# Performance work log

Measured on AMD Instinct MI355X. Metric: run time of the kernel, lower is better.

The kernel has to match this reference:

```python
import jax, jax.numpy as jnp
import numpy as np

B, D, U, C = 2048, 512, 512, 100


def setup_inputs() -> dict:
    key = jax.random.key(0)
    k1, k2, k3 = jax.random.split(key, 3)
    x = jax.random.normal(k1, (B, D), dtype=jnp.float32)
    classes = jax.random.randint(k2, (B, 1), 0, C, dtype=jnp.int64)
    # glorot-uniform-like init for the per-class kernel table
    limit = np.sqrt(6.0 / (D + U)).astype(np.float32)
    kernel = jax.random.uniform(k3, (C, D, U), dtype=jnp.float32, minval=-limit, maxval=limit)
    bias = jnp.zeros((C, U), dtype=jnp.float32)
    return {"x": x, "classes": classes, "kernel": kernel, "bias": bias}


def reference(x, classes, kernel, bias):
    cls = jnp.squeeze(classes, axis=1)            # [B]
    w = kernel[cls]                               # [B, D, U] per-sample gathered kernel
    out = jnp.einsum('bd,bdu->bu', x, w)          # batched matmul, x treated as [B,1,D]
    out = out + bias[cls]                         # per-sample gathered bias
    return out                                    # activation is None (linear)
```

## Files before the change

### kernel.cpp

```cpp
#include <hip/hip_runtime.h>
#include <hip/hip_bf16.h>


typedef __attribute__((ext_vector_type(8))) short bf16x8;
typedef __attribute__((ext_vector_type(4))) short short4v;
typedef __attribute__((ext_vector_type(4))) float floatx4;

constexpr int C_CLS   = 100;
constexpr int B_N     = 2048;
constexpr int D_DIM   = 512;
constexpr int U_DIM   = 512;
constexpr int S_CHUNK = 32;
constexpr int MAX_CHUNKS = 164;
constexpr int TU      = 128;
constexpr int PROWS   = 16;
constexpr int PIECES  = D_DIM / PROWS;
constexpr int NQ      = 4;
constexpr int NWG     = 4 * MAX_CHUNKS;

__device__ __forceinline__ short f2bf(float f) {
    return (short)__builtin_bit_cast(unsigned short, __float2bfloat16(f));
}


__global__ void k_sort(const int* __restrict__ cls, int* __restrict__ order,
                       int* __restrict__ total_chunks, int* __restrict__ chunk_cls,
                       int* __restrict__ chunk_start, int* __restrict__ chunk_len) {
    __shared__ int s_cnt[128], s_off[128], s_chk[128], s_cur[128], s_base[128];
    int tid = threadIdx.x;
    if (tid < 128) s_cnt[tid] = 0;
    __syncthreads();
    for (int i = tid; i < B_N; i += 1024) atomicAdd(&s_cnt[cls[i]], 1);
    __syncthreads();
    int cnt = 0, nch = 0;
    if (tid < 128) {
        cnt = (tid < C_CLS) ? s_cnt[tid] : 0;
        nch = (cnt + S_CHUNK - 1) / S_CHUNK;
        s_off[tid] = cnt; s_chk[tid] = nch;
    }
    __syncthreads();
    for (int st = 1; st < 128; st <<= 1) {
        int a = 0, b = 0;
        if (tid >= st && tid < 128) { a = s_off[tid - st]; b = s_chk[tid - st]; }
        __syncthreads();
        if (tid < 128) { s_off[tid] += a; s_chk[tid] += b; }
        __syncthreads();
    }
    if (tid < C_CLS) {
        int off = s_off[tid] - cnt;
        int cb  = s_chk[tid] - nch;
        s_base[tid] = off;
        s_cur[tid]  = 0;
        for (int j = 0; j < nch; ++j) {
            chunk_cls[cb + j]   = tid;
            chunk_start[cb + j] = off + j * S_CHUNK;
            chunk_len[cb + j]   = min(S_CHUNK, cnt - j * S_CHUNK);
        }
    }
    if (tid == 127) *total_chunks = s_chk[127];
    __syncthreads();
    for (int i = tid; i < B_N; i += 1024) {
        int c = cls[i];
        int p = atomicAdd(&s_cur[c], 1);
        order[s_base[c] + p] = i;
    }
}


#define ISSUE(pi, qq) do {                                                    \
    const int db_ = (pi) * PROWS;                                             \
    _Pragma("unroll")                                                         \
    for (int j_ = 0; j_ < 2; ++j_) {                                          \
        const int r_  = wv * 4 + 2 * j_;           \
        const int rr_ = r_ + (lane >> 5);        \
        const float* gp_ = Wg + (size_t)(db_ + rr_) * U_DIM                   \
                           + (((lane & 31) ^ (rr_ & 15)) << 2);               \
        __builtin_amdgcn_global_load_lds(                                     \
            (const __attribute__((address_space(1))) void*)gp_,               \
            (__attribute__((address_space(3))) void*)&wbuf[qq][r_][0],        \
            16, 0, 0);                                                        \
    }                                                                         \
} while (0)

#define COMPUTE(pi, qq) do {                                                  \
    bf16x8 a8_0, a8_1;                                                        \
    {                                                                         \
        const int xb_ = ((pi) * 32 + g4 * 8) ^ sxw_;                          \
        short4v a4 = *reinterpret_cast<const short4v*>(                       \
            (const char*)xsb + sA * 1024 + xb_);                              \
        a8_0[0]=a4[0]; a8_0[1]=a4[1]; a8_0[2]=a4[2]; a8_0[3]=a4[3];           \
        a8_0[4]=a4[0]; a8_0[5]=a4[1]; a8_0[6]=a4[2]; a8_0[7]=a4[3];           \
        short4v a4b = *reinterpret_cast<const short4v*>(                      \
            (const char*)xsb + (16 + sA) * 1024 + xb_);                       \
        a8_1[0]=a4b[0]; a8_1[1]=a4b[1]; a8_1[2]=a4b[2]; a8_1[3]=a4b[3];       \
        a8_1[4]=a4b[0]; a8_1[5]=a4b[1]; a8_1[6]=a4b[2]; a8_1[7]=a4b[3];       \
    }                                                                         \
    const char* wb_ = (const char*)wbuf + (qq) * (PROWS * TU * 4);            \
    _Pragma("unroll")                                                         \
    for (int nt = 0; nt < 2; ++nt) {                                          \
        const int cb4_ = ((wv << 5) + nt * 16 + sA) << 2;                     \
        bf16x8 b8;                                                            \
        _Pragma("unroll")                                                     \
        for (int j_ = 0; j_ < 4; ++j_) {                                      \
            const int rl_ = g4 * 4 + j_;                                      \
            float w_ = *reinterpret_cast<const float*>(                       \
                wb_ + rl_ * 512 + (cb4_ ^ (rl_ << 4)));                       \
            b8[j_] = f2bf(w_);                                                \
        }                                                                     \
        b8[4] = 0; b8[5] = 0; b8[6] = 0; b8[7] = 0;                           \
        acc0[nt] = __builtin_amdgcn_mfma_f32_16x16x32_bf16(a8_0, b8, acc0[nt], 0, 0, 0); \
        acc1[nt] = __builtin_amdgcn_mfma_f32_16x16x32_bf16(a8_1, b8, acc1[nt], 0, 0, 0); \
    }                                                                         \
} while (0)

#define STEP(pi, NCNT) do {                                                   \
    asm volatile("s_waitcnt vmcnt(" #NCNT ")" ::: "memory");                  \
    __builtin_amdgcn_s_barrier();                  \
    COMPUTE(pi, (pi) & 3);                                                    \
    asm volatile("" ::: "memory");                                            \
    __builtin_amdgcn_s_barrier();               \
    if ((pi) + NQ < PIECES) ISSUE((pi) + NQ, (pi) & 3);                       \
} while (0)

__launch_bounds__(256, 2)
__global__ void k_main(const float* __restrict__ x, const float* __restrict__ kern,
                       const float* __restrict__ bias, const int* __restrict__ order,
                       const int* __restrict__ total_chunks,
                       const int* __restrict__ chunk_cls,
                       const int* __restrict__ chunk_start,
                       const int* __restrict__ chunk_len,
                       float* __restrict__ out) {
    int tc = *total_chunks;
    int A  = 4 * tc;
    int xc = blockIdx.x & 7;
    int ii = blockIdx.x >> 3;
    int q  = A >> 3, r = A & 7;
    int mycnt = (xc < r) ? (q + 1) : q;
    if (ii >= mycnt) return;
    int g = ((xc < r) ? xc * (q + 1) : r * (q + 1) + (xc - r) * q) + ii;

    int chunk = g >> 2;
    int ytile = g & 3;

    int tid  = threadIdx.x;
    int lane = tid & 63;
    int wv   = tid >> 6;
    int sA   = lane & 15;
    int g4   = lane >> 4;
    const int sxw_ = (sA & 7) << 4;

    int c     = chunk_cls[chunk];
    int start = chunk_start[chunk];
    int len   = chunk_len[chunk];
    int u0    = ytile * TU;

    __shared__ float          wbuf[NQ][PROWS][TU];
    __shared__ unsigned short xsb[S_CHUNK][D_DIM];
    __shared__ int            sidx[S_CHUNK];

    const float* Wg = kern + (size_t)c * (D_DIM * U_DIM) + u0;

    if (tid < S_CHUNK) sidx[tid] = (tid < len) ? order[start + tid] : -1;
    asm volatile("s_waitcnt lgkmcnt(0)" ::: "memory");
    __builtin_amdgcn_s_barrier();

    float4 xv0[8], xv1[8];
    int srow0 = (tid >> 4), srow1 = 16 + (tid >> 4);
    int cb    = (tid & 15) * 32;
    {
        int b0 = sidx[srow0]; if (b0 < 0) b0 = sidx[0];
        int b1 = sidx[srow1]; if (b1 < 0) b1 = sidx[0];
        #pragma unroll
        for (int j = 0; j < 8; ++j)
            xv0[j] = reinterpret_cast<const float4*>(x + (size_t)b0 * D_DIM + cb)[j];
        #pragma unroll
        for (int j = 0; j < 8; ++j)
            xv1[j] = reinterpret_cast<const float4*>(x + (size_t)b1 * D_DIM + cb)[j];
    }
    ISSUE(0, 0);
    ISSUE(1, 1);
    ISSUE(2, 2);
    ISSUE(3, 3);
    asm volatile("s_waitcnt vmcnt(8)" ::: "memory");

    {
        #pragma unroll
        for (int p = 0; p < 2; ++p) {
            int   row  = p ? srow1 : srow0;
            char* xrow = (char*)xsb + row * 1024;
            int   swz  = (row & 7) << 4;
            #pragma unroll
            for (int m = 0; m < 4; ++m) {
                float4 va = p ? xv1[2*m]     : xv0[2*m];
                float4 vb = p ? xv1[2*m + 1] : xv0[2*m + 1];
                bf16x8 pk;
                pk[0] = f2bf(va.x); pk[1] = f2bf(va.y);
                pk[2] = f2bf(va.z); pk[3] = f2bf(va.w);
                pk[4] = f2bf(vb.x); pk[5] = f2bf(vb.y);
                pk[6] = f2bf(vb.z); pk[7] = f2bf(vb.w);
                *reinterpret_cast<bf16x8*>(xrow + ((cb * 2 + m * 16) ^ swz)) = pk;
            }
        }
    }
    asm volatile("s_waitcnt lgkmcnt(0)" ::: "memory");
    __builtin_amdgcn_s_barrier();

    floatx4 acc0[2], acc1[2];
    #pragma unroll
    for (int k = 0; k < 2; ++k) {
        acc0[k] = (floatx4){0.f, 0.f, 0.f, 0.f};
        acc1[k] = (floatx4){0.f, 0.f, 0.f, 0.f};
    }

    #pragma unroll 1
    for (int i = 0; i <= 27; ++i) STEP(i, 6);
    STEP(28, 6);
    STEP(29, 4);
    STEP(30, 2);
    STEP(31, 0);

    #pragma unroll
    for (int mt = 0; mt < 2; ++mt) {
        #pragma unroll
        for (int nt = 0; nt < 2; ++nt) {
            int u  = u0 + (wv << 5) + nt * 16 + sA;
            float bb = bias[c * U_DIM + u];
            floatx4 a = mt ? acc1[nt] : acc0[nt];
            #pragma unroll
            for (int r2 = 0; r2 < 4; ++r2) {
                int b = sidx[mt * 16 + g4 * 4 + r2];
                if (b >= 0) out[(size_t)b * U_DIM + u] = a[r2] + bb;
            }
        }
    }
}


extern "C" void kernel_launch(void* const* d_in, const int* in_sizes, int n_in,
                              void* d_out, int out_size, void* d_ws, size_t ws_size,
                              hipStream_t stream) {
    const float* x    = (const float*)d_in[0];
    const int*   cls  = (const int*)d_in[1];
    const float* kern = (const float*)d_in[2];
    const float* bias = (const float*)d_in[3];
    float*       out  = (float*)d_out;

    int* ws           = (int*)d_ws;
    int* order        = ws;
    int* total_chunks = ws + 2048;
    int* chunk_cls    = ws + 2112;
    int* chunk_start  = ws + 2304;
    int* chunk_len    = ws + 2496;

    hipLaunchKernelGGL(k_sort, dim3(1), dim3(1024), 0, stream,
                       cls, order, total_chunks, chunk_cls, chunk_start, chunk_len);
    hipLaunchKernelGGL(k_main, dim3(NWG), dim3(256), 0, stream,
                       x, kern, bias, order, total_chunks, chunk_cls, chunk_start, chunk_len, out);
}
```

Measured before the change: 32.41 us.

## Halve U tile to 64 columns, doubling workgroups and raising occupancy

The U tile per workgroup shrinks from 128 to 64 columns, so there are twice as many workgroups per chunk (8 instead of 4) and each wave computes one 16-column MFMA tile instead of two. Weight staging now issues one 16-byte global-to-LDS load per thread per piece without the XOR swizzle, and the vmcnt waits are adjusted to match. The x-row gather is restructured to load and convert one row-half at a time, and launch bounds move to 3 blocks per CU. The intent is more parallelism and occupancy on a bandwidth-bound gather-GEMM. The cost is redundant x loading and conversion per workgroup, and possible LDS bank conflicts from dropping the swizzle.

```diff
diff --git a/kernel.cpp b/kernel.cpp
--- a/kernel.cpp
+++ b/kernel.cpp
@@ -12,11 +12,11 @@
 constexpr int U_DIM   = 512;
 constexpr int S_CHUNK = 32;
 constexpr int MAX_CHUNKS = 164;
-constexpr int TU      = 128;
+constexpr int TU      = 64;
 constexpr int PROWS   = 16;
 constexpr int PIECES  = D_DIM / PROWS;
 constexpr int NQ      = 4;
-constexpr int NWG     = 4 * MAX_CHUNKS;
+constexpr int NWG     = 8 * MAX_CHUNKS;
 
 __device__ __forceinline__ short f2bf(float f) {
     return (short)__builtin_bit_cast(unsigned short, __float2bfloat16(f));
@@ -68,18 +68,13 @@
 
 
 #define ISSUE(pi, qq) do {                                                    \
-    const int db_ = (pi) * PROWS;                                             \
-    _Pragma("unroll")                                                         \
-    for (int j_ = 0; j_ < 2; ++j_) {                                          \
-        const int r_  = wv * 4 + 2 * j_;           \
-        const int rr_ = r_ + (lane >> 5);        \
-        const float* gp_ = Wg + (size_t)(db_ + rr_) * U_DIM                   \
-                           + (((lane & 31) ^ (rr_ & 15)) << 2);               \
-        __builtin_amdgcn_global_load_lds(                                     \
-            (const __attribute__((address_space(1))) void*)gp_,               \
-            (__attribute__((address_space(3))) void*)&wbuf[qq][r_][0],        \
-            16, 0, 0);                                                        \
-    }                                                                         \
+    const int db_ = (pi) * PROWS + 4 * wv;                                    \
+    const float* gp_ = Wg + (size_t)(db_ + (lane >> 4)) * U_DIM               \
+                       + ((lane & 15) << 2);                                  \
+    __builtin_amdgcn_global_load_lds(                                         \
+        (const __attribute__((address_space(1))) void*)gp_,                   \
+        (__attribute__((address_space(3))) void*)&wbuf[qq][4 * wv][0],        \
+        16, 0, 0);                                                            \
 } while (0)
 
 #define COMPUTE(pi, qq) do {                                                  \
@@ -96,20 +91,18 @@
         a8_1[4]=a4b[0]; a8_1[5]=a4b[1]; a8_1[6]=a4b[2]; a8_1[7]=a4b[3];       \
     }                                                                         \
     const char* wb_ = (const char*)wbuf + (qq) * (PROWS * TU * 4);            \
-    _Pragma("unroll")                                                         \
-    for (int nt = 0; nt < 2; ++nt) {                                          \
-        const int cb4_ = ((wv << 5) + nt * 16 + sA) << 2;                     \
+    {                                                                         \
+        const int cb4_ = (wv * 16 + sA) << 2;      \
         bf16x8 b8;                                                            \
         _Pragma("unroll")                                                     \
         for (int j_ = 0; j_ < 4; ++j_) {                                      \
             const int rl_ = g4 * 4 + j_;                                      \
-            float w_ = *reinterpret_cast<const float*>(                       \
-                wb_ + rl_ * 512 + (cb4_ ^ (rl_ << 4)));                       \
+            float w_ = *reinterpret_cast<const float*>(wb_ + rl_ * 256 + cb4_); \
             b8[j_] = f2bf(w_);                                                \
         }                                                                     \
         b8[4] = 0; b8[5] = 0; b8[6] = 0; b8[7] = 0;                           \
-        acc0[nt] = __builtin_amdgcn_mfma_f32_16x16x32_bf16(a8_0, b8, acc0[nt], 0, 0, 0); \
-        acc1[nt] = __builtin_amdgcn_mfma_f32_16x16x32_bf16(a8_1, b8, acc1[nt], 0, 0, 0); \
+        acc0 = __builtin_amdgcn_mfma_f32_16x16x32_bf16(a8_0, b8, acc0, 0, 0, 0); \
+        acc1 = __builtin_amdgcn_mfma_f32_16x16x32_bf16(a8_1, b8, acc1, 0, 0, 0); \
     }                                                                         \
 } while (0)
 
@@ -122,7 +115,7 @@
     if ((pi) + NQ < PIECES) ISSUE((pi) + NQ, (pi) & 3);                       \
 } while (0)
 
-__launch_bounds__(256, 2)
+__launch_bounds__(256, 3)
 __global__ void k_main(const float* __restrict__ x, const float* __restrict__ kern,
                        const float* __restrict__ bias, const int* __restrict__ order,
                        const int* __restrict__ total_chunks,
@@ -131,7 +124,7 @@
                        const int* __restrict__ chunk_len,
                        float* __restrict__ out) {
     int tc = *total_chunks;
-    int A  = 4 * tc;
+    int A  = 8 * tc;
     int xc = blockIdx.x & 7;
     int ii = blockIdx.x >> 3;
     int q  = A >> 3, r = A & 7;
@@ -139,8 +132,8 @@
     if (ii >= mycnt) return;
     int g = ((xc < r) ? xc * (q + 1) : r * (q + 1) + (xc - r) * q) + ii;
 
-    int chunk = g >> 2;
-    int ytile = g & 3;
+    int chunk = g >> 3;
+    int ytile = g & 7;
 
     int tid  = threadIdx.x;
     int lane = tid & 63;
@@ -164,73 +157,54 @@
     asm volatile("s_waitcnt lgkmcnt(0)" ::: "memory");
     __builtin_amdgcn_s_barrier();
 
-    float4 xv0[8], xv1[8];
-    int srow0 = (tid >> 4), srow1 = 16 + (tid >> 4);
-    int cb    = (tid & 15) * 32;
-    {
-        int b0 = sidx[srow0]; if (b0 < 0) b0 = sidx[0];
-        int b1 = sidx[srow1]; if (b1 < 0) b1 = sidx[0];
-        #pragma unroll
-        for (int j = 0; j < 8; ++j)
-            xv0[j] = reinterpret_cast<const float4*>(x + (size_t)b0 * D_DIM + cb)[j];
-        #pragma unroll
-        for (int j = 0; j < 8; ++j)
-            xv1[j] = reinterpret_cast<const float4*>(x + (size_t)b1 * D_DIM + cb)[j];
-    }
+    int srow = tid >> 4;
+    int cb   = (tid & 15) * 32;
     ISSUE(0, 0);
     ISSUE(1, 1);
     ISSUE(2, 2);
     ISSUE(3, 3);
-    asm volatile("s_waitcnt vmcnt(8)" ::: "memory");
-
-    {
+    #pragma unroll
+    for (int p = 0; p < 2; ++p) {
+        int row = p * 16 + srow;
+        int b0 = sidx[row]; if (b0 < 0) b0 = sidx[0];
+        float4 xv[8];
         #pragma unroll
-        for (int p = 0; p < 2; ++p) {
-            int   row  = p ? srow1 : srow0;
-            char* xrow = (char*)xsb + row * 1024;
-            int   swz  = (row & 7) << 4;
-            #pragma unroll
-            for (int m = 0; m < 4; ++m) {
-                float4 va = p ? xv1[2*m]     : xv0[2*m];
-                float4 vb = p ? xv1[2*m + 1] : xv0[2*m + 1];
-                bf16x8 pk;
-                pk[0] = f2bf(va.x); pk[1] = f2bf(va.y);
-                pk[2] = f2bf(va.z); pk[3] = f2bf(va.w);
-                pk[4] = f2bf(vb.x); pk[5] = f2bf(vb.y);
-                pk[6] = f2bf(vb.z); pk[7] = f2bf(vb.w);
-                *reinterpret_cast<bf16x8*>(xrow + ((cb * 2 + m * 16) ^ swz)) = pk;
-            }
+        for (int j = 0; j < 8; ++j)
+            xv[j] = reinterpret_cast<const float4*>(x + (size_t)b0 * D_DIM + cb)[j];
+        asm volatile("s_waitcnt vmcnt(4)" ::: "memory");
+        char* xrow = (char*)xsb + row * 1024;
+        int   swz  = (row & 7) << 4;
+        #pragma unroll
+        for (int m = 0; m < 4; ++m) {
+            bf16x8 pk;
+            pk[0] = f2bf(xv[2*m].x);   pk[1] = f2bf(xv[2*m].y);
+            pk[2] = f2bf(xv[2*m].z);   pk[3] = f2bf(xv[2*m].w);
+            pk[4] = f2bf(xv[2*m+1].x); pk[5] = f2bf(xv[2*m+1].y);
+            pk[6] = f2bf(xv[2*m+1].z); pk[7] = f2bf(xv[2*m+1].w);
+            *reinterpret_cast<bf16x8*>(xrow + ((cb * 2 + m * 16) ^ swz)) = pk;
         }
     }
     asm volatile("s_waitcnt lgkmcnt(0)" ::: "memory");
     __builtin_amdgcn_s_barrier();
 
-    floatx4 acc0[2], acc1[2];
-    #pragma unroll
-    for (int k = 0; k < 2; ++k) {
-        acc0[k] = (floatx4){0.f, 0.f, 0.f, 0.f};
-        acc1[k] = (floatx4){0.f, 0.f, 0.f, 0.f};
-    }
+    floatx4 acc0 = (floatx4){0.f, 0.f, 0.f, 0.f};
+    floatx4 acc1 = (floatx4){0.f, 0.f, 0.f, 0.f};
 
     #pragma unroll 1
-    for (int i = 0; i <= 27; ++i) STEP(i, 6);
-    STEP(28, 6);
-    STEP(29, 4);
-    STEP(30, 2);
+    for (int i = 0; i <= 28; ++i) STEP(i, 3);
+    STEP(29, 2);
+    STEP(30, 1);
     STEP(31, 0);
 
-    #pragma unroll
-    for (int mt = 0; mt < 2; ++mt) {
+    {
+        int u  = u0 + wv * 16 + sA;
+        float bb = bias[c * U_DIM + u];
         #pragma unroll
-        for (int nt = 0; nt < 2; ++nt) {
-            int u  = u0 + (wv << 5) + nt * 16 + sA;
-            float bb = bias[c * U_DIM + u];
-            floatx4 a = mt ? acc1[nt] : acc0[nt];
-            #pragma unroll
-            for (int r2 = 0; r2 < 4; ++r2) {
-                int b = sidx[mt * 16 + g4 * 4 + r2];
-                if (b >= 0) out[(size_t)b * U_DIM + u] = a[r2] + bb;
-            }
+        for (int r2 = 0; r2 < 4; ++r2) {
+            int b0 = sidx[g4 * 4 + r2];
+            if (b0 >= 0) out[(size_t)b0 * U_DIM + u] = acc0[r2] + bb;
+            int b1 = sidx[16 + g4 * 4 + r2];
+            if (b1 >= 0) out[(size_t)b1 * U_DIM + u] = acc1[r2] + bb;
         }
     }
 }
```

Result: slower. 48.49 us (+49.6%).

## Widen output tile to 256 columns with 512-thread workgroups

Applied to the files above, without the earlier changes.

Doubles the per-workgroup U tile from 128 to 256 columns and the block size from 256 to 512 threads, which halves the number of workgroups per chunk. Each workgroup now gathers and converts the x rows for its chunk once for twice as many output columns, so x loads and bf16 conversion are repeated less often. The LDS weight-staging layout and swizzle are reworked for the wider rows. The costs are a larger LDS footprint, one resident block per CU under the new launch bounds, and fewer workgroups to spread across the GPU.

```diff
diff --git a/kernel.cpp b/kernel.cpp
--- a/kernel.cpp
+++ b/kernel.cpp
@@ -12,11 +12,11 @@
 constexpr int U_DIM   = 512;
 constexpr int S_CHUNK = 32;
 constexpr int MAX_CHUNKS = 164;
-constexpr int TU      = 128;
+constexpr int TU      = 256;
 constexpr int PROWS   = 16;
 constexpr int PIECES  = D_DIM / PROWS;
 constexpr int NQ      = 4;
-constexpr int NWG     = 4 * MAX_CHUNKS;
+constexpr int NWG     = 2 * MAX_CHUNKS;
 
 __device__ __forceinline__ short f2bf(float f) {
     return (short)__builtin_bit_cast(unsigned short, __float2bfloat16(f));
@@ -71,13 +71,12 @@
     const int db_ = (pi) * PROWS;                                             \
     _Pragma("unroll")                                                         \
     for (int j_ = 0; j_ < 2; ++j_) {                                          \
-        const int r_  = wv * 4 + 2 * j_;           \
-        const int rr_ = r_ + (lane >> 5);        \
-        const float* gp_ = Wg + (size_t)(db_ + rr_) * U_DIM                   \
-                           + (((lane & 31) ^ (rr_ & 15)) << 2);               \
+        const int row_ = 2 * wv + j_;                                         \
+        const float* gp_ = Wg + (size_t)(db_ + row_) * U_DIM                  \
+                           + ((lane ^ (row_ & 7)) << 2);                      \
         __builtin_amdgcn_global_load_lds(                                     \
             (const __attribute__((address_space(1))) void*)gp_,               \
-            (__attribute__((address_space(3))) void*)&wbuf[qq][r_][0],        \
+            (__attribute__((address_space(3))) void*)&wbuf[qq][row_][0],      \
             16, 0, 0);                                                        \
     }                                                                         \
 } while (0)
@@ -98,13 +97,13 @@
     const char* wb_ = (const char*)wbuf + (qq) * (PROWS * TU * 4);            \
     _Pragma("unroll")                                                         \
     for (int nt = 0; nt < 2; ++nt) {                                          \
-        const int cb4_ = ((wv << 5) + nt * 16 + sA) << 2;                     \
+        const int c_ = (wv << 5) + nt * 16 + sA;        \
         bf16x8 b8;                                                            \
         _Pragma("unroll")                                                     \
         for (int j_ = 0; j_ < 4; ++j_) {                                      \
             const int rl_ = g4 * 4 + j_;                                      \
             float w_ = *reinterpret_cast<const float*>(                       \
-                wb_ + rl_ * 512 + (cb4_ ^ (rl_ << 4)));                       \
+                wb_ + rl_ * 1024 + ((c_ << 2) ^ ((rl_ & 7) << 4)));           \
             b8[j_] = f2bf(w_);                                                \
         }                                                                     \
         b8[4] = 0; b8[5] = 0; b8[6] = 0; b8[7] = 0;                           \
@@ -115,14 +114,14 @@
 
 #define STEP(pi, NCNT) do {                                                   \
     asm volatile("s_waitcnt vmcnt(" #NCNT ")" ::: "memory");                  \
-    __builtin_amdgcn_s_barrier();                  \
+    __builtin_amdgcn_s_barrier();                                             \
     COMPUTE(pi, (pi) & 3);                                                    \
     asm volatile("" ::: "memory");                                            \
-    __builtin_amdgcn_s_barrier();               \
+    __builtin_amdgcn_s_barrier();                                             \
     if ((pi) + NQ < PIECES) ISSUE((pi) + NQ, (pi) & 3);                       \
 } while (0)
 
-__launch_bounds__(256, 2)
+__launch_bounds__(512, 1)
 __global__ void k_main(const float* __restrict__ x, const float* __restrict__ kern,
                        const float* __restrict__ bias, const int* __restrict__ order,
                        const int* __restrict__ total_chunks,
@@ -131,7 +130,7 @@
                        const int* __restrict__ chunk_len,
                        float* __restrict__ out) {
     int tc = *total_chunks;
-    int A  = 4 * tc;
+    int A  = 2 * tc;
     int xc = blockIdx.x & 7;
     int ii = blockIdx.x >> 3;
     int q  = A >> 3, r = A & 7;
@@ -139,8 +138,8 @@
     if (ii >= mycnt) return;
     int g = ((xc < r) ? xc * (q + 1) : r * (q + 1) + (xc - r) * q) + ii;
 
-    int chunk = g >> 2;
-    int ytile = g & 3;
+    int chunk = g >> 1;
+    int ytile = g & 1;
 
     int tid  = threadIdx.x;
     int lane = tid & 63;
@@ -164,18 +163,14 @@
     asm volatile("s_waitcnt lgkmcnt(0)" ::: "memory");
     __builtin_amdgcn_s_barrier();
 
-    float4 xv0[8], xv1[8];
-    int srow0 = (tid >> 4), srow1 = 16 + (tid >> 4);
-    int cb    = (tid & 15) * 32;
+    int srow = tid >> 4;
+    int cb   = (tid & 15) * 32;
+    float4 xv[8];
     {
-        int b0 = sidx[srow0]; if (b0 < 0) b0 = sidx[0];
-        int b1 = sidx[srow1]; if (b1 < 0) b1 = sidx[0];
+        int b0 = sidx[srow]; if (b0 < 0) b0 = sidx[0];
         #pragma unroll
         for (int j = 0; j < 8; ++j)
-            xv0[j] = reinterpret_cast<const float4*>(x + (size_t)b0 * D_DIM + cb)[j];
-        #pragma unroll
-        for (int j = 0; j < 8; ++j)
-            xv1[j] = reinterpret_cast<const float4*>(x + (size_t)b1 * D_DIM + cb)[j];
+            xv[j] = reinterpret_cast<const float4*>(x + (size_t)b0 * D_DIM + cb)[j];
     }
     ISSUE(0, 0);
     ISSUE(1, 1);
@@ -184,22 +179,16 @@
     asm volatile("s_waitcnt vmcnt(8)" ::: "memory");
 
     {
+        char* xrow = (char*)xsb + srow * 1024;
+        int   swz  = (srow & 7) << 4;
         #pragma unroll
-        for (int p = 0; p < 2; ++p) {
-            int   row  = p ? srow1 : srow0;
-            char* xrow = (char*)xsb + row * 1024;
-            int   swz  = (row & 7) << 4;
-            #pragma unroll
-            for (int m = 0; m < 4; ++m) {
-                float4 va = p ? xv1[2*m]     : xv0[2*m];
-                float4 vb = p ? xv1[2*m + 1] : xv0[2*m + 1];
-                bf16x8 pk;
-                pk[0] = f2bf(va.x); pk[1] = f2bf(va.y);
-                pk[2] = f2bf(va.z); pk[3] = f2bf(va.w);
-                pk[4] = f2bf(vb.x); pk[5] = f2bf(vb.y);
-                pk[6] = f2bf(vb.z); pk[7] = f2bf(vb.w);
-                *reinterpret_cast<bf16x8*>(xrow + ((cb * 2 + m * 16) ^ swz)) = pk;
-            }
+        for (int m = 0; m < 4; ++m) {
+            bf16x8 pk;
+            pk[0] = f2bf(xv[2*m].x);   pk[1] = f2bf(xv[2*m].y);
+            pk[2] = f2bf(xv[2*m].z);   pk[3] = f2bf(xv[2*m].w);
+            pk[4] = f2bf(xv[2*m+1].x); pk[5] = f2bf(xv[2*m+1].y);
+            pk[6] = f2bf(xv[2*m+1].z); pk[7] = f2bf(xv[2*m+1].w);
+            *reinterpret_cast<bf16x8*>(xrow + ((cb * 2 + m * 16) ^ swz)) = pk;
         }
     }
     asm volatile("s_waitcnt lgkmcnt(0)" ::: "memory");
@@ -254,6 +243,6 @@
 
     hipLaunchKernelGGL(k_sort, dim3(1), dim3(1024), 0, stream,
                        cls, order, total_chunks, chunk_cls, chunk_start, chunk_len);
-    hipLaunchKernelGGL(k_main, dim3(NWG), dim3(256), 0, stream,
+    hipLaunchKernelGGL(k_main, dim3(NWG), dim3(512), 0, stream,
                        x, kern, bias, order, total_chunks, chunk_cls, chunk_start, chunk_len, out);
 }
```

Measured after the change: 33.25 us. 1.03x slower.
